# Optimization experiments

Hardware: AMD Instinct MI355X
Metric: run time of the kernel (lower is better)

## Reference

```python
import jax, jax.numpy as jnp
import numpy as np

N, M, D, DV = 8192, 8192, 128, 128

def setup_inputs() -> dict:
    key = jax.random.key(0)
    kq, kk, kv = jax.random.split(key, 3)
    return {
        "Q": jax.random.normal(kq, (N, D), dtype=jnp.float32),
        "K": jax.random.normal(kk, (M, D), dtype=jnp.float32),
        "V": jax.random.normal(kv, (M, DV), dtype=jnp.float32),
    }

def reference(Q, K, V):
    # scores: [N, M] = Q @ K^T (no 1/sqrt(d) scaling, matching the source)
    scores = jnp.einsum("nd,md->nm", Q, K)
    attention_weights = jax.nn.softmax(scores, axis=1)  # softmax over keys
    return jnp.einsum("nm,mv->nv", attention_weights, V)  # [N, DV]
```

## Files before the change

kernel.cpp:

```cpp
#include <hip/hip_runtime.h>
#include <hip/hip_bf16.h>

#define NQ   8192
#define NKEY 8192
#define DH   128

#define BQ   128
#define BK   64
#define BUFB 32768
#define LOG2E 1.44269504088896340736f

typedef __attribute__((ext_vector_type(8)))  short    short8;
typedef __attribute__((ext_vector_type(4)))  short    short4v;
typedef _Float16 half8 __attribute__((ext_vector_type(8)));
typedef __attribute__((ext_vector_type(16))) float    f32x16;
typedef __attribute__((ext_vector_type(4)))  float    float4v;

union BFU { __hip_bfloat16 b; unsigned short u; };
__device__ __forceinline__ unsigned short f2bf(float x) { BFU u; u.b = __float2bfloat16(x); return u.u; }

__device__ __forceinline__ void full_drain_barrier() {
    __builtin_amdgcn_s_waitcnt(0);
    __syncthreads();
}

__global__ void prep(const float* __restrict__ K, const float* __restrict__ V,
                     _Float16* __restrict__ Kh, unsigned short* __restrict__ Vt) {
    __shared__ __attribute__((aligned(16))) unsigned short tile[64 * 72];
    int b = blockIdx.x;
    int t = threadIdx.x;
    if (b < 512) {
        int idx = (b * 256 + t) * 8;
        float4v x0 = *(const float4v*)(K + idx);
        float4v x1 = *(const float4v*)(K + idx + 4);
        half8 o;
#pragma unroll
        for (int j = 0; j < 4; ++j) { o[j] = (_Float16)x0[j]; o[4 + j] = (_Float16)x1[j]; }
        *(half8*)(Kh + idx) = o;
    } else {
        int tv = b - 512;
        int m0 = (tv >> 1) * 64, n0 = (tv & 1) * 64;
#pragma unroll
        for (int it = 0; it < 4; ++it) {
            int id = t + it * 256;
            int mm = id >> 4, nn0 = (id & 15) * 4;
            int mmP = (mm & ~12) | ((mm & 4) << 1) | ((mm & 8) >> 1);
            float4v x = *(const float4v*)(V + (size_t)(m0 + mm) * DH + n0 + nn0);
#pragma unroll
            for (int j = 0; j < 4; ++j)
                tile[(nn0 + j) * 72 + mmP] = f2bf(x[j]);
        }
        __syncthreads();
        int nn = t >> 2, ch = t & 3;
        *(short8*)(Vt + (size_t)(n0 + nn) * NKEY + m0 + ch * 16)     = *(const short8*)&tile[nn * 72 + ch * 16];
        *(short8*)(Vt + (size_t)(n0 + nn) * NKEY + m0 + ch * 16 + 8) = *(const short8*)&tile[nn * 72 + ch * 16 + 8];
    }
}

__launch_bounds__(256, 2)
__global__ void attn_fwd(const float* __restrict__ Q,
                         const _Float16* __restrict__ Kh,
                         const unsigned short* __restrict__ Vt,
                         unsigned short* __restrict__ Opart, float* __restrict__ lpart,
                         float* __restrict__ out, int KS) {
    __shared__ __attribute__((aligned(16))) char sbuf[2 * BUFB];

    const int tid  = threadIdx.x;
    const int lane = tid & 63;
    const int w    = tid >> 6;
    const int l31  = lane & 31;
    const int h    = lane >> 5;

    const int s  = blockIdx.x % KS;
    const int qb = blockIdx.x / KS;
    const int mlen   = NKEY / KS;
    const int kbase  = s * mlen;
    const int ntiles = mlen / BK;

    const char* gbase[8]; int mult[8]; int ldsoff[8];
#pragma unroll
    for (int i = 0; i < 8; ++i) {
        int Lb = w * 512 + i * 64;
        int L  = Lb + lane;
        const char* gb; int mu;
        if (Lb < 1024) { int r = L >> 4, cg = (L & 15) ^ (r & 15);
                         gb = (const char*)Kh + r * 256 + cg * 16; mu = 256; }
        else           { int Lv = L - 1024; int n = Lv >> 3, cg = (Lv & 7) ^ (n & 7);
                         gb = (const char*)Vt + (size_t)n * (NKEY * 2) + cg * 16; mu = 2; }
        gbase[i] = gb; mult[i] = mu; ldsoff[i] = Lb * 16;
    }

    const int qrow = qb * BQ + w * 32 + l31;
    half8 qf[8];
#pragma unroll
    for (int c = 0; c < 8; ++c) {
        const float* qp = Q + (size_t)qrow * DH + c * 16 + h * 8;
        float4v x0 = *(const float4v*)qp;
        float4v x1 = *(const float4v*)(qp + 4);
#pragma unroll
        for (int i = 0; i < 4; ++i) {
            qf[c][i]     = (_Float16)(x0[i] * LOG2E);
            qf[c][4 + i] = (_Float16)(x1[i] * LOG2E);
        }
    }

    int koff[8];
#pragma unroll
    for (int c = 0; c < 8; ++c)
        koff[c] = l31 * 256 + (((c * 2 + h) ^ (l31 & 15)) << 4);
    int voff[4];
#pragma unroll
    for (int c2 = 0; c2 < 4; ++c2)
        voff[c2] = 16384 + l31 * 128 + (((c2 * 2 + h) ^ (l31 & 7)) << 4);

    float lsum = 0.0f;
    f32x16 O[4];
#pragma unroll
    for (int ct = 0; ct < 4; ++ct)
#pragma unroll
        for (int r = 0; r < 16; ++r) O[ct][r] = 0.0f;

    auto stage = [&](int t, int bufbyte) {
        int kb = kbase + t * BK;
#pragma unroll
        for (int i = 0; i < 8; ++i) {
            const char* g = gbase[i] + (size_t)kb * mult[i];
            __builtin_amdgcn_global_load_lds(
                (const __attribute__((address_space(1))) unsigned int*)g,
                (__attribute__((address_space(3))) unsigned int*)(sbuf + bufbyte + ldsoff[i]),
                16, 0, 0);
        }
    };

    auto compute_tile = [&](int BUF) {
        const char* bp = sbuf + BUF;
        f32x16 S0, S1;
#pragma unroll
        for (int r = 0; r < 16; ++r) { S0[r] = 0.0f; S1[r] = 0.0f; }
#pragma unroll
        for (int c = 0; c < 8; ++c) {
            half8 k0 = *(const half8*)(bp + koff[c]);
            half8 k1 = *(const half8*)(bp + koff[c] + 8192);
            S0 = __builtin_amdgcn_mfma_f32_32x32x16_f16(k0, qf[c], S0, 0, 0, 0);
            S1 = __builtin_amdgcn_mfma_f32_32x32x16_f16(k1, qf[c], S1, 0, 0, 0);
        }
        union PU { unsigned int u[4]; short8 s8; } B0, B1, B2, B3;
        {
            short8 va0[4], va1[4];
#pragma unroll
            for (int ct = 0; ct < 4; ++ct) {
                va0[ct] = *(const short8*)(bp + voff[0] + ct * 4096);
                va1[ct] = *(const short8*)(bp + voff[1] + ct * 4096);
            }
            float p0[16]; float ps = 0.0f;
#pragma unroll
            for (int r = 0; r < 16; ++r) { p0[r] = __builtin_amdgcn_exp2f(S0[r]); ps += p0[r]; }
            lsum += ps;
#pragma unroll
            for (int j = 0; j < 4; ++j) {
                B0.u[j] = __builtin_amdgcn_perm(__float_as_uint(p0[2*j+1]), __float_as_uint(p0[2*j]),   0x07060302u);
                B1.u[j] = __builtin_amdgcn_perm(__float_as_uint(p0[2*j+9]), __float_as_uint(p0[2*j+8]), 0x07060302u);
            }
#pragma unroll
            for (int ct = 0; ct < 4; ++ct) {
                O[ct] = __builtin_amdgcn_mfma_f32_32x32x16_bf16(va0[ct], B0.s8, O[ct], 0, 0, 0);
                O[ct] = __builtin_amdgcn_mfma_f32_32x32x16_bf16(va1[ct], B1.s8, O[ct], 0, 0, 0);
            }
        }
        {
            short8 va2[4], va3[4];
#pragma unroll
            for (int ct = 0; ct < 4; ++ct) {
                va2[ct] = *(const short8*)(bp + voff[2] + ct * 4096);
                va3[ct] = *(const short8*)(bp + voff[3] + ct * 4096);
            }
            float p1[16]; float ps = 0.0f;
#pragma unroll
            for (int r = 0; r < 16; ++r) { p1[r] = __builtin_amdgcn_exp2f(S1[r]); ps += p1[r]; }
            lsum += ps;
#pragma unroll
            for (int j = 0; j < 4; ++j) {
                B2.u[j] = __builtin_amdgcn_perm(__float_as_uint(p1[2*j+1]), __float_as_uint(p1[2*j]),   0x07060302u);
                B3.u[j] = __builtin_amdgcn_perm(__float_as_uint(p1[2*j+9]), __float_as_uint(p1[2*j+8]), 0x07060302u);
            }
#pragma unroll
            for (int ct = 0; ct < 4; ++ct) {
                O[ct] = __builtin_amdgcn_mfma_f32_32x32x16_bf16(va2[ct], B2.s8, O[ct], 0, 0, 0);
                O[ct] = __builtin_amdgcn_mfma_f32_32x32x16_bf16(va3[ct], B3.s8, O[ct], 0, 0, 0);
            }
        }
    };

    stage(0, 0);
    for (int t = 0; t < ntiles; t += 2) {
        full_drain_barrier();
        stage(t + 1, BUFB);
        compute_tile(0);
        full_drain_barrier();
        if (t + 2 < ntiles) stage(t + 2, 0);
        compute_tile(BUFB);
    }

    lsum += __shfl_xor(lsum, 32, 64);
    {
        unsigned short* Ob = Opart + ((size_t)s * NQ + qrow) * DH;
#pragma unroll
        for (int ct = 0; ct < 4; ++ct)
#pragma unroll
            for (int g = 0; g < 4; ++g) {
                short4v v;
#pragma unroll
                for (int j = 0; j < 4; ++j) v[j] = (short)f2bf(O[ct][4 * g + j]);
                *(short4v*)(Ob + ct * 32 + 8 * g + 4 * h) = v;
            }
        if (h == 0)
            lpart[(size_t)s * NQ + qrow] = lsum;
    }
}

__global__ void attn_combine(const unsigned short* __restrict__ Opart,
                             const float* __restrict__ lpart, float* __restrict__ out, int KS) {
    int idx = blockIdx.x * 256 + threadIdx.x;
    int row = idx >> 5;
    int col = (idx & 31) << 2;
    float den = 0.0f;
    float a0 = 0.0f, a1 = 0.0f, a2 = 0.0f, a3 = 0.0f;
    for (int s2 = 0; s2 < KS; ++s2) {
        den += lpart[(size_t)s2 * NQ + row];
        const unsigned short* op = Opart + ((size_t)s2 * NQ + row) * DH + col;
        uint2 u = *(const uint2*)op;
        a0 += __uint_as_float(u.x << 16);
        a1 += __uint_as_float(u.x & 0xffff0000u);
        a2 += __uint_as_float(u.y << 16);
        a3 += __uint_as_float(u.y & 0xffff0000u);
    }
    float r = 1.0f / den;
    float4v v; v[0] = a0 * r; v[1] = a1 * r; v[2] = a2 * r; v[3] = a3 * r;
    *(float4v*)(out + (size_t)row * DH + col) = v;
}

extern "C" void kernel_launch(void* const* d_in, const int* in_sizes, int n_in,
                              void* d_out, int out_size, void* d_ws, size_t ws_size,
                              hipStream_t stream) {
    const float* Q = (const float*)d_in[0];
    const float* K = (const float*)d_in[1];
    const float* V = (const float*)d_in[2];
    float* out = (float*)d_out;

    const size_t prep_bytes = 2 * (size_t)NKEY * DH * sizeof(unsigned short);
    int KS = 8;
    while (KS > 1 &&
           ws_size < prep_bytes + (size_t)KS * ((size_t)NQ * DH * 2 + NQ * 4))
        KS >>= 1;

    _Float16* Kh = (_Float16*)d_ws;
    unsigned short* Vt = (unsigned short*)(Kh + (size_t)NKEY * DH);
    unsigned short* Opart = Vt + (size_t)NKEY * DH;
    float* lpart = (float*)(Opart + (size_t)KS * NQ * DH);

    hipLaunchKernelGGL(prep, dim3(768), dim3(256), 0, stream, K, V, Kh, Vt);
    hipLaunchKernelGGL(attn_fwd, dim3((NQ / BQ) * KS), dim3(256), 0, stream,
                       Q, Kh, Vt, Opart, lpart, out, KS);
    hipLaunchKernelGGL(attn_combine, dim3((NQ * DH) / 4 / 256), dim3(256), 0, stream,
                       Opart, lpart, out, KS);
}
```

Before: 115.1 us.

## Fuse split-K combine into attention kernel via last-block atomic counter

Removes the separate combine kernel launch. Each query block's split-K workers increment a per-query-block atomic counter after writing partials, and the last arriver reduces the KS partial outputs and writes the final result. This saves a kernel launch and its gap, but adds a fence, an atomic and a serialized tail reduction done by one block per query tile. Counters are zeroed in the prep kernel.

```diff
diff --git a/kernel.cpp b/kernel.cpp
--- a/kernel.cpp
+++ b/kernel.cpp
@@ -25,10 +25,12 @@
 }
 
 __global__ void prep(const float* __restrict__ K, const float* __restrict__ V,
-                     _Float16* __restrict__ Kh, unsigned short* __restrict__ Vt) {
+                     _Float16* __restrict__ Kh, unsigned short* __restrict__ Vt,
+                     unsigned int* __restrict__ qcnt) {
     __shared__ __attribute__((aligned(16))) unsigned short tile[64 * 72];
     int b = blockIdx.x;
     int t = threadIdx.x;
+    if (b == 0 && t < 64) qcnt[t] = 0;
     if (b < 512) {
         int idx = (b * 256 + t) * 8;
         float4v x0 = *(const float4v*)(K + idx);
@@ -62,6 +64,7 @@
                          const _Float16* __restrict__ Kh,
                          const unsigned short* __restrict__ Vt,
                          unsigned short* __restrict__ Opart, float* __restrict__ lpart,
+                         unsigned int* __restrict__ qcnt,
                          float* __restrict__ out, int KS) {
     __shared__ __attribute__((aligned(16))) char sbuf[2 * BUFB];
 
@@ -216,27 +219,38 @@
         if (h == 0)
             lpart[(size_t)s * NQ + qrow] = lsum;
     }
-}
-
-__global__ void attn_combine(const unsigned short* __restrict__ Opart,
-                             const float* __restrict__ lpart, float* __restrict__ out, int KS) {
-    int idx = blockIdx.x * 256 + threadIdx.x;
-    int row = idx >> 5;
-    int col = (idx & 31) << 2;
-    float den = 0.0f;
-    float a0 = 0.0f, a1 = 0.0f, a2 = 0.0f, a3 = 0.0f;
-    for (int s2 = 0; s2 < KS; ++s2) {
-        den += lpart[(size_t)s2 * NQ + row];
-        const unsigned short* op = Opart + ((size_t)s2 * NQ + row) * DH + col;
-        uint2 u = *(const uint2*)op;
-        a0 += __uint_as_float(u.x << 16);
-        a1 += __uint_as_float(u.x & 0xffff0000u);
-        a2 += __uint_as_float(u.y << 16);
-        a3 += __uint_as_float(u.y & 0xffff0000u);
-    }
-    float r = 1.0f / den;
-    float4v v; v[0] = a0 * r; v[1] = a1 * r; v[2] = a2 * r; v[3] = a3 * r;
-    *(float4v*)(out + (size_t)row * DH + col) = v;
+
+    __syncthreads();
+    unsigned int* sh = (unsigned int*)sbuf;
+    if (tid == 0) {
+        __threadfence();
+        sh[0] = __hip_atomic_fetch_add(&qcnt[qb], 1u, __ATOMIC_ACQ_REL,
+                                       __HIP_MEMORY_SCOPE_AGENT);
+    }
+    __syncthreads();
+    if (sh[0] == (unsigned int)(KS - 1)) {
+        const int base = qb * BQ * (DH / 4);
+#pragma unroll 4
+        for (int i = 0; i < BQ * (DH / 4) / 256; ++i) {
+            int idx = base + i * 256 + tid;
+            int row = idx >> 5;
+            int col = (idx & 31) << 2;
+            float den = 0.0f;
+            float a0 = 0.0f, a1 = 0.0f, a2 = 0.0f, a3 = 0.0f;
+            for (int s2 = 0; s2 < KS; ++s2) {
+                den += lpart[(size_t)s2 * NQ + row];
+                const unsigned short* op = Opart + ((size_t)s2 * NQ + row) * DH + col;
+                uint2 u = *(const uint2*)op;
+                a0 += __uint_as_float(u.x << 16);
+                a1 += __uint_as_float(u.x & 0xffff0000u);
+                a2 += __uint_as_float(u.y << 16);
+                a3 += __uint_as_float(u.y & 0xffff0000u);
+            }
+            float rr = 1.0f / den;
+            float4v vv; vv[0] = a0 * rr; vv[1] = a1 * rr; vv[2] = a2 * rr; vv[3] = a3 * rr;
+            *(float4v*)(out + (size_t)row * DH + col) = vv;
+        }
+    }
 }
 
 extern "C" void kernel_launch(void* const* d_in, const int* in_sizes, int n_in,
@@ -250,17 +264,16 @@
     const size_t prep_bytes = 2 * (size_t)NKEY * DH * sizeof(unsigned short);
     int KS = 8;
     while (KS > 1 &&
-           ws_size < prep_bytes + (size_t)KS * ((size_t)NQ * DH * 2 + NQ * 4))
+           ws_size < prep_bytes + (size_t)KS * ((size_t)NQ * DH * 2 + NQ * 4) + 256)
         KS >>= 1;
 
     _Float16* Kh = (_Float16*)d_ws;
     unsigned short* Vt = (unsigned short*)(Kh + (size_t)NKEY * DH);
     unsigned short* Opart = Vt + (size_t)NKEY * DH;
     float* lpart = (float*)(Opart + (size_t)KS * NQ * DH);
-
-    hipLaunchKernelGGL(prep, dim3(768), dim3(256), 0, stream, K, V, Kh, Vt);
+    unsigned int* qcnt = (unsigned int*)(lpart + (size_t)KS * NQ);
+
+    hipLaunchKernelGGL(prep, dim3(768), dim3(256), 0, stream, K, V, Kh, Vt, qcnt);
     hipLaunchKernelGGL(attn_fwd, dim3((NQ / BQ) * KS), dim3(256), 0, stream,
-                       Q, Kh, Vt, Opart, lpart, out, KS);
-    hipLaunchKernelGGL(attn_combine, dim3((NQ * DH) / 4 / 256), dim3(256), 0, stream,
-                       Opart, lpart, out, KS);
-}
+                       Q, Kh, Vt, Opart, lpart, qcnt, out, KS);
+}
```

After: 179.4 us. 1.56x slower.

## Split K/V staging with double-buffered K and single V buffer, raise occupancy

Applied to the files above, without the earlier changes.

Restructures the attention loop so K tiles are double-buffered and prefetched one tile ahead, while V occupies a single buffer that is refilled after the PV MMAs. A partial vmcnt wait replaces the full drain barrier. LDS drops from 64KB to 48KB, which allows the launch bound of 3 blocks per CU, and the key-split factor goes from 8 to 16 for more blocks. The trade-offs are more partial outputs to combine, tighter register limits, and V loads that are less hidden because V has no double buffer.

```diff
diff --git a/kernel.cpp b/kernel.cpp
--- a/kernel.cpp
+++ b/kernel.cpp
@@ -7,7 +7,7 @@
 
 #define BQ   128
 #define BK   64
-#define BUFB 32768
+#define VBUF 32768
 #define LOG2E 1.44269504088896340736f
 
 typedef __attribute__((ext_vector_type(8)))  short    short8;
@@ -18,11 +18,6 @@
 
 union BFU { __hip_bfloat16 b; unsigned short u; };
 __device__ __forceinline__ unsigned short f2bf(float x) { BFU u; u.b = __float2bfloat16(x); return u.u; }
-
-__device__ __forceinline__ void full_drain_barrier() {
-    __builtin_amdgcn_s_waitcnt(0);
-    __syncthreads();
-}
 
 __global__ void prep(const float* __restrict__ K, const float* __restrict__ V,
                      _Float16* __restrict__ Kh, unsigned short* __restrict__ Vt) {
@@ -57,13 +52,13 @@
     }
 }
 
-__launch_bounds__(256, 2)
+__launch_bounds__(256, 3)
 __global__ void attn_fwd(const float* __restrict__ Q,
                          const _Float16* __restrict__ Kh,
                          const unsigned short* __restrict__ Vt,
                          unsigned short* __restrict__ Opart, float* __restrict__ lpart,
-                         float* __restrict__ out, int KS) {
-    __shared__ __attribute__((aligned(16))) char sbuf[2 * BUFB];
+                         int KS) {
+    __shared__ __attribute__((aligned(16))) char sbuf[49152];
 
     const int tid  = threadIdx.x;
     const int lane = tid & 63;
@@ -77,18 +72,40 @@
     const int kbase  = s * mlen;
     const int ntiles = mlen / BK;
 
-    const char* gbase[8]; int mult[8]; int ldsoff[8];
-#pragma unroll
-    for (int i = 0; i < 8; ++i) {
-        int Lb = w * 512 + i * 64;
-        int L  = Lb + lane;
-        const char* gb; int mu;
-        if (Lb < 1024) { int r = L >> 4, cg = (L & 15) ^ (r & 15);
-                         gb = (const char*)Kh + r * 256 + cg * 16; mu = 256; }
-        else           { int Lv = L - 1024; int n = Lv >> 3, cg = (Lv & 7) ^ (n & 7);
-                         gb = (const char*)Vt + (size_t)n * (NKEY * 2) + cg * 16; mu = 2; }
-        gbase[i] = gb; mult[i] = mu; ldsoff[i] = Lb * 16;
-    }
+    const char* gbK[4]; int ldsK[4];
+    const char* gbV[4]; int ldsV[4];
+#pragma unroll
+    for (int i = 0; i < 4; ++i) {
+        int L = w * 256 + i * 64 + lane;
+        int r  = L >> 4, cgk = (L & 15) ^ (r & 15);
+        gbK[i]  = (const char*)Kh + r * 256 + cgk * 16;
+        ldsK[i] = (w * 256 + i * 64) * 16;
+        int n  = L >> 3, cgv = (L & 7) ^ (n & 7);
+        gbV[i]  = (const char*)Vt + (size_t)n * (NKEY * 2) + cgv * 16;
+        ldsV[i] = VBUF + (w * 256 + i * 64) * 16;
+    }
+
+    auto stageK = [&](int t, int kpar) {
+        int kb = kbase + t * BK;
+#pragma unroll
+        for (int i = 0; i < 4; ++i)
+            __builtin_amdgcn_global_load_lds(
+                (const __attribute__((address_space(1))) unsigned int*)(gbK[i] + (size_t)kb * 256),
+                (__attribute__((address_space(3))) unsigned int*)(sbuf + kpar * 16384 + ldsK[i]),
+                16, 0, 0);
+    };
+    auto stageV = [&](int t) {
+        int kb = kbase + t * BK;
+#pragma unroll
+        for (int i = 0; i < 4; ++i)
+            __builtin_amdgcn_global_load_lds(
+                (const __attribute__((address_space(1))) unsigned int*)(gbV[i] + (size_t)kb * 2),
+                (__attribute__((address_space(3))) unsigned int*)(sbuf + ldsV[i]),
+                16, 0, 0);
+    };
+
+    stageK(0, 0);
+    stageV(0);
 
     const int qrow = qb * BQ + w * 32 + l31;
     half8 qf[8];
@@ -111,7 +128,7 @@
     int voff[4];
 #pragma unroll
     for (int c2 = 0; c2 < 4; ++c2)
-        voff[c2] = 16384 + l31 * 128 + (((c2 * 2 + h) ^ (l31 & 7)) << 4);
+        voff[c2] = VBUF + l31 * 128 + (((c2 * 2 + h) ^ (l31 & 7)) << 4);
 
     float lsum = 0.0f;
     f32x16 O[4];
@@ -120,38 +137,24 @@
 #pragma unroll
         for (int r = 0; r < 16; ++r) O[ct][r] = 0.0f;
 
-    auto stage = [&](int t, int bufbyte) {
-        int kb = kbase + t * BK;
-#pragma unroll
-        for (int i = 0; i < 8; ++i) {
-            const char* g = gbase[i] + (size_t)kb * mult[i];
-            __builtin_amdgcn_global_load_lds(
-                (const __attribute__((address_space(1))) unsigned int*)g,
-                (__attribute__((address_space(3))) unsigned int*)(sbuf + bufbyte + ldsoff[i]),
-                16, 0, 0);
-        }
-    };
-
-    auto compute_tile = [&](int BUF) {
-        const char* bp = sbuf + BUF;
+    __syncthreads();
+
+    for (int t = 0; t < ntiles; ++t) {
+        const char* kb_ = sbuf + (t & 1) * 16384;
+        if (t + 1 < ntiles) stageK(t + 1, (t + 1) & 1);
+
         f32x16 S0, S1;
 #pragma unroll
         for (int r = 0; r < 16; ++r) { S0[r] = 0.0f; S1[r] = 0.0f; }
 #pragma unroll
         for (int c = 0; c < 8; ++c) {
-            half8 k0 = *(const half8*)(bp + koff[c]);
-            half8 k1 = *(const half8*)(bp + koff[c] + 8192);
+            half8 k0 = *(const half8*)(kb_ + koff[c]);
+            half8 k1 = *(const half8*)(kb_ + koff[c] + 8192);
             S0 = __builtin_amdgcn_mfma_f32_32x32x16_f16(k0, qf[c], S0, 0, 0, 0);
             S1 = __builtin_amdgcn_mfma_f32_32x32x16_f16(k1, qf[c], S1, 0, 0, 0);
         }
         union PU { unsigned int u[4]; short8 s8; } B0, B1, B2, B3;
         {
-            short8 va0[4], va1[4];
-#pragma unroll
-            for (int ct = 0; ct < 4; ++ct) {
-                va0[ct] = *(const short8*)(bp + voff[0] + ct * 4096);
-                va1[ct] = *(const short8*)(bp + voff[1] + ct * 4096);
-            }
             float p0[16]; float ps = 0.0f;
 #pragma unroll
             for (int r = 0; r < 16; ++r) { p0[r] = __builtin_amdgcn_exp2f(S0[r]); ps += p0[r]; }
@@ -161,19 +164,8 @@
                 B0.u[j] = __builtin_amdgcn_perm(__float_as_uint(p0[2*j+1]), __float_as_uint(p0[2*j]),   0x07060302u);
                 B1.u[j] = __builtin_amdgcn_perm(__float_as_uint(p0[2*j+9]), __float_as_uint(p0[2*j+8]), 0x07060302u);
             }
-#pragma unroll
-            for (int ct = 0; ct < 4; ++ct) {
-                O[ct] = __builtin_amdgcn_mfma_f32_32x32x16_bf16(va0[ct], B0.s8, O[ct], 0, 0, 0);
-                O[ct] = __builtin_amdgcn_mfma_f32_32x32x16_bf16(va1[ct], B1.s8, O[ct], 0, 0, 0);
-            }
-        }
-        {
-            short8 va2[4], va3[4];
-#pragma unroll
-            for (int ct = 0; ct < 4; ++ct) {
-                va2[ct] = *(const short8*)(bp + voff[2] + ct * 4096);
-                va3[ct] = *(const short8*)(bp + voff[3] + ct * 4096);
-            }
+        }
+        {
             float p1[16]; float ps = 0.0f;
 #pragma unroll
             for (int r = 0; r < 16; ++r) { p1[r] = __builtin_amdgcn_exp2f(S1[r]); ps += p1[r]; }
@@ -183,22 +175,41 @@
                 B2.u[j] = __builtin_amdgcn_perm(__float_as_uint(p1[2*j+1]), __float_as_uint(p1[2*j]),   0x07060302u);
                 B3.u[j] = __builtin_amdgcn_perm(__float_as_uint(p1[2*j+9]), __float_as_uint(p1[2*j+8]), 0x07060302u);
             }
+        }
+
+        if (t + 1 < ntiles) { asm volatile("s_waitcnt vmcnt(4)" ::: "memory"); }
+        else                { asm volatile("s_waitcnt vmcnt(0)" ::: "memory"); }
+        __builtin_amdgcn_s_barrier();
+
+        {
+            short8 va0[4], va1[4];
+#pragma unroll
+            for (int ct = 0; ct < 4; ++ct) {
+                va0[ct] = *(const short8*)(sbuf + voff[0] + ct * 4096);
+                va1[ct] = *(const short8*)(sbuf + voff[1] + ct * 4096);
+            }
+#pragma unroll
+            for (int ct = 0; ct < 4; ++ct) {
+                O[ct] = __builtin_amdgcn_mfma_f32_32x32x16_bf16(va0[ct], B0.s8, O[ct], 0, 0, 0);
+                O[ct] = __builtin_amdgcn_mfma_f32_32x32x16_bf16(va1[ct], B1.s8, O[ct], 0, 0, 0);
+            }
+        }
+        {
+            short8 va2[4], va3[4];
+#pragma unroll
+            for (int ct = 0; ct < 4; ++ct) {
+                va2[ct] = *(const short8*)(sbuf + voff[2] + ct * 4096);
+                va3[ct] = *(const short8*)(sbuf + voff[3] + ct * 4096);
+            }
 #pragma unroll
             for (int ct = 0; ct < 4; ++ct) {
                 O[ct] = __builtin_amdgcn_mfma_f32_32x32x16_bf16(va2[ct], B2.s8, O[ct], 0, 0, 0);
                 O[ct] = __builtin_amdgcn_mfma_f32_32x32x16_bf16(va3[ct], B3.s8, O[ct], 0, 0, 0);
             }
         }
-    };
-
-    stage(0, 0);
-    for (int t = 0; t < ntiles; t += 2) {
-        full_drain_barrier();
-        stage(t + 1, BUFB);
-        compute_tile(0);
-        full_drain_barrier();
-        if (t + 2 < ntiles) stage(t + 2, 0);
-        compute_tile(BUFB);
+
+        __syncthreads();
+        if (t + 1 < ntiles) stageV(t + 1);
     }
 
     lsum += __shfl_xor(lsum, 32, 64);
@@ -248,7 +259,7 @@
     float* out = (float*)d_out;
 
     const size_t prep_bytes = 2 * (size_t)NKEY * DH * sizeof(unsigned short);
-    int KS = 8;
+    int KS = 16;
     while (KS > 1 &&
            ws_size < prep_bytes + (size_t)KS * ((size_t)NQ * DH * 2 + NQ * 4))
         KS >>= 1;
@@ -260,7 +271,7 @@
 
     hipLaunchKernelGGL(prep, dim3(768), dim3(256), 0, stream, K, V, Kh, Vt);
     hipLaunchKernelGGL(attn_fwd, dim3((NQ / BQ) * KS), dim3(256), 0, stream,
-                       Q, Kh, Vt, Opart, lpart, out, KS);
+                       Q, Kh, Vt, Opart, lpart, KS);
     hipLaunchKernelGGL(attn_combine, dim3((NQ * DH) / 4 / 256), dim3(256), 0, stream,
                        Opart, lpart, out, KS);
 }
```

New measurement: 136.6 us. +18.6%, slower.
